# Optimization experiments

Hardware: AMD Instinct MI355X
Metric: run time of the kernel (lower is better)

Reference implementation:

```python
import jax, jax.numpy as jnp
import numpy as np

B, S, D, H = 32, 2048, 128, 16  # batch, cached kv len, head dim (=d_model), heads
EPS = 1e-5


def setup_inputs() -> dict:
    key = jax.random.key(0)
    ks = jax.random.split(key, 5)
    d_total = D * H
    x = jax.random.normal(ks[0], (B, 1, D), jnp.float32)
    past_k = jax.random.normal(ks[1], (B, H, S, D), jnp.float32)
    past_v = jax.random.normal(ks[2], (B, H, S, D), jnp.float32)
    Wqkv = jax.random.normal(ks[3], (3 * d_total, D), jnp.float32) * 0.02
    bqkv = jnp.zeros((3 * d_total,), jnp.float32)
    Wout = jax.random.normal(ks[4], (D, d_total), jnp.float32) * 0.02
    bout = jnp.zeros((D,), jnp.float32)
    return {"x": x, "past_k": past_k, "past_v": past_v,
            "Wqkv": Wqkv, "bqkv": bqkv, "Wout": Wout, "bout": bout}


def reference(x, past_k, past_v, Wqkv, bqkv, Wout, bout):
    # QKV projection: (B,1,D) -> (B,1,3*H*D)
    qkv = x @ Wqkv.T + bqkv
    qkv = qkv.reshape(B, 1, 3 * H, D).transpose(0, 2, 1, 3)  # (B,3H,1,D)
    q, k_new, v_new = jnp.split(qkv, 3, axis=1)              # each (B,H,1,D)
    k = jnp.concatenate([past_k, k_new], axis=2)             # (B,H,S+1,D)
    v = jnp.concatenate([past_v, v_new], axis=2)
    # single-query attention (causal mask is trivially all-visible for q_len=1)
    scale = 1.0 / jnp.sqrt(jnp.float32(D))
    scores = jnp.einsum('bhqd,bhkd->bhqk', q, k) * scale     # (B,H,1,S+1)
    probs = jax.nn.softmax(scores, axis=-1)
    y = jnp.einsum('bhqk,bhkd->bhqd', probs, v)              # (B,H,1,D)
    y = y.transpose(0, 2, 1, 3).reshape(B, 1, H * D)         # (B,1,H*D)
    y = y @ Wout.T + bout                                    # (B,1,D)
    y = y + x                                                # residual
    # layer norm over last dim, no affine params
    mu = jnp.mean(y, axis=-1, keepdims=True)
    var = jnp.mean(jnp.square(y - mu), axis=-1, keepdims=True)
    out = (y - mu) / jnp.sqrt(var + EPS)
    return (out, k, v)
```

## Files before the change

kernel.cpp:

```cpp
#include <hip/hip_runtime.h>
#include <math.h>

#define B 32
#define S 2048
#define S1 2049
#define D 128
#define H 16
#define DT 2048
#define EPS 1e-5f
#define SCALE 0.08838834764831845f

__global__ void __launch_bounds__(256)
qkv_proj_kernel(const float* __restrict__ x,
                const float* __restrict__ Wqkv,
                const float* __restrict__ bqkv,
                float* __restrict__ qkv) {
    const int b = blockIdx.x;
    const int j = blockIdx.y * 256 + threadIdx.x;
    __shared__ float xs[D];
    if (threadIdx.x < D) xs[threadIdx.x] = x[b * D + threadIdx.x];
    __syncthreads();
    const float* w = Wqkv + (size_t)j * D;
    float acc = bqkv[j];
#pragma unroll
    for (int d = 0; d < D; d += 4) {
        float4 w4 = *reinterpret_cast<const float4*>(w + d);
        acc = fmaf(w4.x, xs[d + 0], acc);
        acc = fmaf(w4.y, xs[d + 1], acc);
        acc = fmaf(w4.z, xs[d + 2], acc);
        acc = fmaf(w4.w, xs[d + 3], acc);
    }
    qkv[(size_t)b * (3 * DT) + j] = acc;
}

__global__ void __launch_bounds__(256)
attn_kernel(const float* __restrict__ past_k,
            const float* __restrict__ past_v,
            const float* __restrict__ qkv,
            float* __restrict__ out_k,
            float* __restrict__ out_v,
            float* __restrict__ yh) {
    const int bh = blockIdx.x;
    const int b = bh / H;
    const int h = bh % H;
    const int tid  = threadIdx.x;
    const int wave = tid >> 6;
    const int lane = tid & 63;
    const int half = lane >> 5;
    const int l32  = lane & 31;
    const int rg   = wave * 2 + half;

    __shared__ float sc[S1];
    __shared__ float rbuf[256];
    __shared__ float red[8 * D];

    const float* qp   = qkv + (size_t)b * (3 * DT) + (size_t)h * D;
    const float* knew = qkv + (size_t)b * (3 * DT) + (size_t)(H + h) * D;
    const float* vnew = qkv + (size_t)b * (3 * DT) + (size_t)(2 * H + h) * D;

    const float4 q4 = reinterpret_cast<const float4*>(qp)[l32];

    const float* kin  = past_k + (size_t)(b * H + h) * S  * D;
    const float* vin  = past_v + (size_t)(b * H + h) * S  * D;
    float*       kout = out_k  + (size_t)(b * H + h) * S1 * D;
    float*       vout = out_v  + (size_t)(b * H + h) * S1 * D;

    for (int s = rg; s < S1; s += 8) {
        float4 k4;
        if (s < S) k4 = reinterpret_cast<const float4*>(kin + (size_t)s * D)[l32];
        else       k4 = reinterpret_cast<const float4*>(knew)[l32];
        reinterpret_cast<float4*>(kout + (size_t)s * D)[l32] = k4;
        float p = q4.x * k4.x + q4.y * k4.y + q4.z * k4.z + q4.w * k4.w;
        p += __shfl_xor(p, 1);
        p += __shfl_xor(p, 2);
        p += __shfl_xor(p, 4);
        p += __shfl_xor(p, 8);
        p += __shfl_xor(p, 16);
        if (l32 == 0) sc[s] = p * SCALE;
    }
    __syncthreads();

    float m = -1e30f;
    for (int i = tid; i < S1; i += 256) m = fmaxf(m, sc[i]);
    rbuf[tid] = m;
    __syncthreads();
    for (int off = 128; off > 0; off >>= 1) {
        if (tid < off) rbuf[tid] = fmaxf(rbuf[tid], rbuf[tid + off]);
        __syncthreads();
    }
    m = rbuf[0];
    __syncthreads();

    float lsum = 0.f;
    for (int i = tid; i < S1; i += 256) {
        float e = expf(sc[i] - m);
        sc[i] = e;
        lsum += e;
    }
    rbuf[tid] = lsum;
    __syncthreads();
    for (int off = 128; off > 0; off >>= 1) {
        if (tid < off) rbuf[tid] += rbuf[tid + off];
        __syncthreads();
    }
    const float inv = 1.0f / rbuf[0];
    __syncthreads();

    float4 acc = make_float4(0.f, 0.f, 0.f, 0.f);
    for (int s = rg; s < S1; s += 8) {
        float4 v4;
        if (s < S) v4 = reinterpret_cast<const float4*>(vin + (size_t)s * D)[l32];
        else       v4 = reinterpret_cast<const float4*>(vnew)[l32];
        reinterpret_cast<float4*>(vout + (size_t)s * D)[l32] = v4;
        const float p = sc[s];
        acc.x = fmaf(p, v4.x, acc.x);
        acc.y = fmaf(p, v4.y, acc.y);
        acc.z = fmaf(p, v4.z, acc.z);
        acc.w = fmaf(p, v4.w, acc.w);
    }
    reinterpret_cast<float4*>(red)[rg * 32 + l32] = acc;
    __syncthreads();

    if (tid < D) {
        float s = 0.f;
#pragma unroll
        for (int g = 0; g < 8; ++g) s += red[g * D + tid];
        yh[(size_t)(b * H + h) * D + tid] = s * inv;
    }
}

__global__ void __launch_bounds__(128)
out_proj_kernel(const float* __restrict__ x,
                const float* __restrict__ yh,
                const float* __restrict__ Wout,
                const float* __restrict__ bout,
                float* __restrict__ out) {
    const int b = blockIdx.x;
    const int d = threadIdx.x;
    __shared__ float ys[DT];
    __shared__ float tb[D];

    for (int j = d; j < DT; j += D) ys[j] = yh[(size_t)b * DT + j];
    __syncthreads();

    const float* w = Wout + (size_t)d * DT;
    float acc = bout[d];
    for (int j = 0; j < DT; j += 4) {
        float4 w4 = *reinterpret_cast<const float4*>(w + j);
        acc = fmaf(w4.x, ys[j + 0], acc);
        acc = fmaf(w4.y, ys[j + 1], acc);
        acc = fmaf(w4.z, ys[j + 2], acc);
        acc = fmaf(w4.w, ys[j + 3], acc);
    }
    acc += x[b * D + d];

    tb[d] = acc;
    __syncthreads();
    for (int off = 64; off > 0; off >>= 1) {
        if (d < off) tb[d] += tb[d + off];
        __syncthreads();
    }
    const float mu = tb[0] * (1.0f / D);
    __syncthreads();
    const float diff = acc - mu;
    tb[d] = diff * diff;
    __syncthreads();
    for (int off = 64; off > 0; off >>= 1) {
        if (d < off) tb[d] += tb[d + off];
        __syncthreads();
    }
    const float var = tb[0] * (1.0f / D);
    out[(size_t)b * D + d] = diff / sqrtf(var + EPS);
}

extern "C" void kernel_launch(void* const* d_in, const int* in_sizes, int n_in,
                              void* d_out, int out_size, void* d_ws, size_t ws_size,
                              hipStream_t stream) {
    const float* x      = (const float*)d_in[0];
    const float* past_k = (const float*)d_in[1];
    const float* past_v = (const float*)d_in[2];
    const float* Wqkv   = (const float*)d_in[3];
    const float* bqkv   = (const float*)d_in[4];
    const float* Wout   = (const float*)d_in[5];
    const float* bout   = (const float*)d_in[6];

    float* out   = (float*)d_out;
    float* out_k = out + (size_t)B * D;
    float* out_v = out_k + (size_t)B * H * S1 * D;

    float* qkv = (float*)d_ws;
    float* yh  = qkv + (size_t)B * 3 * DT;

    qkv_proj_kernel<<<dim3(B, (3 * DT) / 256), 256, 0, stream>>>(x, Wqkv, bqkv, qkv);
    attn_kernel<<<B * H, 256, 0, stream>>>(past_k, past_v, qkv, out_k, out_v, yh);
    out_proj_kernel<<<B, D, 0, stream>>>(x, yh, Wout, bout, out);
}
```

Baseline: 547.0 us.

## Split-KV single-pass online softmax attention with combine fused into out-proj

Attention now runs as a single streaming pass with online softmax instead of three passes through a shared score buffer. The KV length is split four ways across blocks, which raises the grid from 512 to 2048 blocks. Partial max, sum and accumulators are merged in the output-projection kernel, which also handles the new-token score; the new K/V rows are written by the QKV kernel. Loads and stores use nontemporal builtins and the out-proj GEMV is spread over 1024 threads. The risks are extra workspace traffic and rescaling exps in every loop iteration.

```diff
diff --git a/kernel.cpp b/kernel.cpp
--- a/kernel.cpp
+++ b/kernel.cpp
@@ -7,14 +7,20 @@
 #define D 128
 #define H 16
 #define DT 2048
+#define NS 4
+#define ROWS_PER_SPLIT 512
 #define EPS 1e-5f
 #define SCALE 0.08838834764831845f
+
+typedef float f4v __attribute__((ext_vector_type(4)));
 
 __global__ void __launch_bounds__(256)
 qkv_proj_kernel(const float* __restrict__ x,
                 const float* __restrict__ Wqkv,
                 const float* __restrict__ bqkv,
-                float* __restrict__ qkv) {
+                float* __restrict__ qkv,
+                float* __restrict__ out_k,
+                float* __restrict__ out_v) {
     const int b = blockIdx.x;
     const int j = blockIdx.y * 256 + threadIdx.x;
     __shared__ float xs[D];
@@ -31,6 +37,16 @@
         acc = fmaf(w4.w, xs[d + 3], acc);
     }
     qkv[(size_t)b * (3 * DT) + j] = acc;
+
+    if (j >= DT) {
+        const int r = j - DT;
+        const int which = r >> 11;
+        const int hd = r & (DT - 1);
+        const int h = hd >> 7;
+        const int d = hd & 127;
+        float* dst = which ? out_v : out_k;
+        dst[((size_t)(b * H + h) * S1 + S) * D + d] = acc;
+    }
 }
 
 __global__ void __launch_bounds__(256)
@@ -39,10 +55,13 @@
             const float* __restrict__ qkv,
             float* __restrict__ out_k,
             float* __restrict__ out_v,
-            float* __restrict__ yh) {
-    const int bh = blockIdx.x;
-    const int b = bh / H;
-    const int h = bh % H;
+            float* __restrict__ part_ml,
+            float* __restrict__ part_acc) {
+    const int bx = blockIdx.x;
+    const int split = bx & (NS - 1);
+    const int bh = bx >> 2;
+    const int b = bh >> 4;
+    const int h = bh & (H - 1);
     const int tid  = threadIdx.x;
     const int wave = tid >> 6;
     const int lane = tid & 63;
@@ -50,127 +69,165 @@
     const int l32  = lane & 31;
     const int rg   = wave * 2 + half;
 
-    __shared__ float sc[S1];
-    __shared__ float rbuf[256];
-    __shared__ float red[8 * D];
-
-    const float* qp   = qkv + (size_t)b * (3 * DT) + (size_t)h * D;
-    const float* knew = qkv + (size_t)b * (3 * DT) + (size_t)(H + h) * D;
-    const float* vnew = qkv + (size_t)b * (3 * DT) + (size_t)(2 * H + h) * D;
-
-    const float4 q4 = reinterpret_cast<const float4*>(qp)[l32];
-
-    const float* kin  = past_k + (size_t)(b * H + h) * S  * D;
-    const float* vin  = past_v + (size_t)(b * H + h) * S  * D;
-    float*       kout = out_k  + (size_t)(b * H + h) * S1 * D;
-    float*       vout = out_v  + (size_t)(b * H + h) * S1 * D;
-
-    for (int s = rg; s < S1; s += 8) {
-        float4 k4;
-        if (s < S) k4 = reinterpret_cast<const float4*>(kin + (size_t)s * D)[l32];
-        else       k4 = reinterpret_cast<const float4*>(knew)[l32];
-        reinterpret_cast<float4*>(kout + (size_t)s * D)[l32] = k4;
-        float p = q4.x * k4.x + q4.y * k4.y + q4.z * k4.z + q4.w * k4.w;
+    const f4v* __restrict__ kin  = (const f4v*)past_k + (size_t)(b * H + h) * S * 32;
+    const f4v* __restrict__ vin  = (const f4v*)past_v + (size_t)(b * H + h) * S * 32;
+    f4v* __restrict__ kout = (f4v*)out_k + (size_t)(b * H + h) * S1 * 32;
+    f4v* __restrict__ vout = (f4v*)out_v + (size_t)(b * H + h) * S1 * 32;
+
+    const f4v q4 = ((const f4v*)qkv)[(size_t)b * (3 * DT / 4) + h * 32 + l32];
+
+    const int s0 = split * ROWS_PER_SPLIT + rg;
+
+    float m = -1e30f;
+    float l = 0.f;
+    f4v acc = (f4v){0.f, 0.f, 0.f, 0.f};
+
+#pragma unroll 4
+    for (int it = 0; it < ROWS_PER_SPLIT / 8; ++it) {
+        const int s = s0 + it * 8;
+        const size_t off = (size_t)s * 32 + l32;
+        f4v k4 = __builtin_nontemporal_load(&kin[off]);
+        __builtin_nontemporal_store(k4, &kout[off]);
+        f4v t = k4 * q4;
+        float p = t.x + t.y + t.z + t.w;
         p += __shfl_xor(p, 1);
         p += __shfl_xor(p, 2);
         p += __shfl_xor(p, 4);
         p += __shfl_xor(p, 8);
         p += __shfl_xor(p, 16);
-        if (l32 == 0) sc[s] = p * SCALE;
-    }
-    __syncthreads();
-
-    float m = -1e30f;
-    for (int i = tid; i < S1; i += 256) m = fmaxf(m, sc[i]);
-    rbuf[tid] = m;
-    __syncthreads();
-    for (int off = 128; off > 0; off >>= 1) {
-        if (tid < off) rbuf[tid] = fmaxf(rbuf[tid], rbuf[tid + off]);
-        __syncthreads();
-    }
-    m = rbuf[0];
-    __syncthreads();
-
-    float lsum = 0.f;
-    for (int i = tid; i < S1; i += 256) {
-        float e = expf(sc[i] - m);
-        sc[i] = e;
-        lsum += e;
-    }
-    rbuf[tid] = lsum;
-    __syncthreads();
-    for (int off = 128; off > 0; off >>= 1) {
-        if (tid < off) rbuf[tid] += rbuf[tid + off];
-        __syncthreads();
-    }
-    const float inv = 1.0f / rbuf[0];
-    __syncthreads();
-
-    float4 acc = make_float4(0.f, 0.f, 0.f, 0.f);
-    for (int s = rg; s < S1; s += 8) {
-        float4 v4;
-        if (s < S) v4 = reinterpret_cast<const float4*>(vin + (size_t)s * D)[l32];
-        else       v4 = reinterpret_cast<const float4*>(vnew)[l32];
-        reinterpret_cast<float4*>(vout + (size_t)s * D)[l32] = v4;
-        const float p = sc[s];
-        acc.x = fmaf(p, v4.x, acc.x);
-        acc.y = fmaf(p, v4.y, acc.y);
-        acc.z = fmaf(p, v4.z, acc.z);
-        acc.w = fmaf(p, v4.w, acc.w);
-    }
-    reinterpret_cast<float4*>(red)[rg * 32 + l32] = acc;
+        p *= SCALE;
+        f4v v4 = __builtin_nontemporal_load(&vin[off]);
+        __builtin_nontemporal_store(v4, &vout[off]);
+        const float mn = fmaxf(m, p);
+        const float c = __expf(m - mn);
+        const float e = __expf(p - mn);
+        l = l * c + e;
+        acc = acc * c;
+        acc += v4 * e;
+        m = mn;
+    }
+
+    __shared__ float sm[8];
+    __shared__ float sl[8];
+    __shared__ float sacc[8 * D];
+    ((f4v*)sacc)[rg * 32 + l32] = acc;
+    if (l32 == 0) { sm[rg] = m; sl[rg] = l; }
     __syncthreads();
 
     if (tid < D) {
-        float s = 0.f;
-#pragma unroll
-        for (int g = 0; g < 8; ++g) s += red[g * D + tid];
-        yh[(size_t)(b * H + h) * D + tid] = s * inv;
-    }
-}
-
-__global__ void __launch_bounds__(128)
+        float M = sm[0];
+#pragma unroll
+        for (int g = 1; g < 8; ++g) M = fmaxf(M, sm[g]);
+        float L = 0.f, y = 0.f;
+#pragma unroll
+        for (int g = 0; g < 8; ++g) {
+            const float wgt = __expf(sm[g] - M);
+            L += wgt * sl[g];
+            y = fmaf(wgt, sacc[g * D + tid], y);
+        }
+        part_acc[(size_t)bx * D + tid] = y;
+        if (tid == 0) {
+            part_ml[2 * bx + 0] = M;
+            part_ml[2 * bx + 1] = L;
+        }
+    }
+}
+
+__global__ void __launch_bounds__(1024)
 out_proj_kernel(const float* __restrict__ x,
-                const float* __restrict__ yh,
+                const float* __restrict__ qkv,
+                const float* __restrict__ part_ml,
+                const float* __restrict__ part_acc,
                 const float* __restrict__ Wout,
                 const float* __restrict__ bout,
                 float* __restrict__ out) {
     const int b = blockIdx.x;
-    const int d = threadIdx.x;
+    const int t = threadIdx.x;
     __shared__ float ys[DT];
+    __shared__ float pp[D * 8];
     __shared__ float tb[D];
 
-    for (int j = d; j < DT; j += D) ys[j] = yh[(size_t)b * DT + j];
-    __syncthreads();
-
-    const float* w = Wout + (size_t)d * DT;
-    float acc = bout[d];
-    for (int j = 0; j < DT; j += 4) {
-        float4 w4 = *reinterpret_cast<const float4*>(w + j);
-        acc = fmaf(w4.x, ys[j + 0], acc);
-        acc = fmaf(w4.y, ys[j + 1], acc);
-        acc = fmaf(w4.z, ys[j + 2], acc);
-        acc = fmaf(w4.w, ys[j + 3], acc);
-    }
-    acc += x[b * D + d];
-
-    tb[d] = acc;
+    {
+        const int h = t >> 6;
+        const int lane = t & 63;
+        const float* qp   = qkv + (size_t)b * (3 * DT) + h * D;
+        const float* knew = qp + DT;
+        const float* vnew = qp + 2 * DT;
+        float pd = qp[2 * lane] * knew[2 * lane] + qp[2 * lane + 1] * knew[2 * lane + 1];
+        pd += __shfl_xor(pd, 1);
+        pd += __shfl_xor(pd, 2);
+        pd += __shfl_xor(pd, 4);
+        pd += __shfl_xor(pd, 8);
+        pd += __shfl_xor(pd, 16);
+        pd += __shfl_xor(pd, 32);
+        const float s = pd * SCALE;
+
+        const int bh = b * H + h;
+        float m0 = part_ml[2 * (bh * NS + 0)], l0 = part_ml[2 * (bh * NS + 0) + 1];
+        float m1 = part_ml[2 * (bh * NS + 1)], l1 = part_ml[2 * (bh * NS + 1) + 1];
+        float m2 = part_ml[2 * (bh * NS + 2)], l2 = part_ml[2 * (bh * NS + 2) + 1];
+        float m3 = part_ml[2 * (bh * NS + 3)], l3 = part_ml[2 * (bh * NS + 3) + 1];
+        float M = fmaxf(fmaxf(fmaxf(m0, m1), fmaxf(m2, m3)), s);
+        const float w0 = __expf(m0 - M), w1 = __expf(m1 - M);
+        const float w2 = __expf(m2 - M), w3 = __expf(m3 - M);
+        const float wn = __expf(s - M);
+        const float L = w0 * l0 + w1 * l1 + w2 * l2 + w3 * l3 + wn;
+        const float invL = 1.0f / L;
+#pragma unroll
+        for (int r = 0; r < 2; ++r) {
+            const int d = lane + r * 64;
+            float y = wn * vnew[d];
+            y = fmaf(w0, part_acc[(size_t)(bh * NS + 0) * D + d], y);
+            y = fmaf(w1, part_acc[(size_t)(bh * NS + 1) * D + d], y);
+            y = fmaf(w2, part_acc[(size_t)(bh * NS + 2) * D + d], y);
+            y = fmaf(w3, part_acc[(size_t)(bh * NS + 3) * D + d], y);
+            ys[h * D + d] = y * invL;
+        }
+    }
+    __syncthreads();
+
+    {
+        const int d = t >> 3;
+        const int sub = t & 7;
+        const float* w = Wout + (size_t)d * DT + sub * 256;
+        const float* y = ys + sub * 256;
+        float acc = 0.f;
+#pragma unroll
+        for (int j = 0; j < 256; j += 4) {
+            float4 w4 = *reinterpret_cast<const float4*>(w + j);
+            acc = fmaf(w4.x, y[j + 0], acc);
+            acc = fmaf(w4.y, y[j + 1], acc);
+            acc = fmaf(w4.z, y[j + 2], acc);
+            acc = fmaf(w4.w, y[j + 3], acc);
+        }
+        pp[d * 8 + sub] = acc;
+    }
+    __syncthreads();
+
+    float val = 0.f;
+    if (t < D) {
+        float a = 0.f;
+#pragma unroll
+        for (int g = 0; g < 8; ++g) a += pp[t * 8 + g];
+        val = a + bout[t] + x[b * D + t];
+        tb[t] = val;
+    }
     __syncthreads();
     for (int off = 64; off > 0; off >>= 1) {
-        if (d < off) tb[d] += tb[d + off];
+        if (t < off) tb[t] += tb[t + off];
         __syncthreads();
     }
     const float mu = tb[0] * (1.0f / D);
     __syncthreads();
-    const float diff = acc - mu;
-    tb[d] = diff * diff;
+    const float diff = val - mu;
+    if (t < D) tb[t] = diff * diff;
     __syncthreads();
     for (int off = 64; off > 0; off >>= 1) {
-        if (d < off) tb[d] += tb[d + off];
+        if (t < off) tb[t] += tb[t + off];
         __syncthreads();
     }
     const float var = tb[0] * (1.0f / D);
-    out[(size_t)b * D + d] = diff / sqrtf(var + EPS);
+    if (t < D) out[(size_t)b * D + t] = diff / sqrtf(var + EPS);
 }
 
 extern "C" void kernel_launch(void* const* d_in, const int* in_sizes, int n_in,
@@ -188,10 +245,14 @@
     float* out_k = out + (size_t)B * D;
     float* out_v = out_k + (size_t)B * H * S1 * D;
 
-    float* qkv = (float*)d_ws;
-    float* yh  = qkv + (size_t)B * 3 * DT;
-
-    qkv_proj_kernel<<<dim3(B, (3 * DT) / 256), 256, 0, stream>>>(x, Wqkv, bqkv, qkv);
-    attn_kernel<<<B * H, 256, 0, stream>>>(past_k, past_v, qkv, out_k, out_v, yh);
-    out_proj_kernel<<<B, D, 0, stream>>>(x, yh, Wout, bout, out);
-}
+    float* qkv      = (float*)d_ws;
+    float* part_ml  = qkv + (size_t)B * 3 * DT;
+    float* part_acc = part_ml + 2 * B * H * NS;
+
+    qkv_proj_kernel<<<dim3(B, (3 * DT) / 256), 256, 0, stream>>>(
+        x, Wqkv, bqkv, qkv, out_k, out_v);
+    attn_kernel<<<B * H * NS, 256, 0, stream>>>(
+        past_k, past_v, qkv, out_k, out_v, part_ml, part_acc);
+    out_proj_kernel<<<B, 1024, 0, stream>>>(
+        x, qkv, part_ml, part_acc, Wout, bout, out);
+}
```

After: 493.9 us. 1.11x faster.
